# Performance work log

Measured on AMD Instinct MI355X. Metric: run time of the kernel, lower is better.

## Reference

```python
import jax, jax.numpy as jnp
import numpy as np

B = 8192          # batch (tokens)
D_LAT = 1024      # latent_dim
D_EMB = 1024      # embed_dim
D = D_LAT + D_EMB # input_dim = 2048
E = 8             # num_experts
K = 2             # top-k


def setup_inputs() -> dict:
    key = jax.random.key(0)
    ks = jax.random.split(key, 6)
    s = 1.0 / np.sqrt(D)  # PyTorch nn.Linear init bound
    return {
        "x": jax.random.normal(ks[0], (B, D_LAT), dtype=jnp.float32),
        "y": jax.random.normal(ks[1], (B, D_EMB), dtype=jnp.float32),
        # expert Linear weights [E, out=D, in=D] and biases [E, D]
        "W_experts": jax.random.uniform(ks[2], (E, D, D), jnp.float32, -s, s),
        "b_experts": jax.random.uniform(ks[3], (E, D), jnp.float32, -s, s),
        # gate Linear weight [E, D] and bias [E]
        "W_gate": jax.random.uniform(ks[4], (E, D), jnp.float32, -s, s),
        "b_gate": jax.random.uniform(ks[5], (E,), jnp.float32, -s, s),
    }


def reference(x, y, W_experts, b_experts, W_gate, b_gate):
    # inp: [B, D]
    inp = jnp.concatenate([x, y], axis=1)
    # gating (eval mode: no noise): [B, E]
    gate_logits = inp @ W_gate.T + b_gate
    # top-k values/indices (sorted descending, matching torch.topk): [B, K]
    topk_val, topk_idx = jax.lax.top_k(gate_logits, K)
    topk_gates = jax.nn.softmax(topk_val, axis=1)  # [B, K]
    # dense all-expert outputs, matching original per-expert loop: [B, E, D]
    all_out = jnp.einsum('bd,eod->beo', inp, W_experts) + b_experts[None, :, :]
    # gather top-k expert outputs: [B, K, D]
    topk_out = jnp.take_along_axis(all_out, topk_idx[:, :, None], axis=1)
    # gate-weighted combine: [B, D]
    fused = jnp.sum(topk_out * topk_gates[:, :, None], axis=1)
    return fused
```

## Files before the change

kernel.cpp:

```cpp
#include <hip/hip_runtime.h>
#include <stdint.h>

typedef __attribute__((ext_vector_type(4))) float f32x4;
typedef __attribute__((ext_vector_type(8))) short short8v;
typedef __attribute__((ext_vector_type(8))) unsigned short ushort8v;
typedef __attribute__((ext_vector_type(4))) unsigned short ushort4v;

#define NB 8192
#define ND 2048
#define NE 8
#define NT 32

__device__ __forceinline__ unsigned short f2bf(float f) {
    union { float f; uint32_t u; } c; c.f = f;
    uint32_t u = c.u;
    u = u + 0x7FFFu + ((u >> 16) & 1u);
    return (unsigned short)(u >> 16);
}

__global__ __launch_bounds__(256) void cvt_w_kernel(const float* __restrict__ W,
                                                    unsigned short* __restrict__ Wb) {
    size_t i = ((size_t)blockIdx.x * 256 + threadIdx.x) * 8;
    float4 a = *(const float4*)(W + i);
    float4 b = *(const float4*)(W + i + 4);
    ushort8v o;
    o[0] = f2bf(a.x); o[1] = f2bf(a.y); o[2] = f2bf(a.z); o[3] = f2bf(a.w);
    o[4] = f2bf(b.x); o[5] = f2bf(b.y); o[6] = f2bf(b.z); o[7] = f2bf(b.w);
    *(ushort8v*)(Wb + i) = o;
}

__global__ __launch_bounds__(256) void gatecvt_kernel(const float* __restrict__ x,
                                                      const float* __restrict__ y,
                                                      const float* __restrict__ Wg,
                                                      const float* __restrict__ bg,
                                                      unsigned short* __restrict__ inpb,
                                                      int* __restrict__ tkidx,
                                                      float* __restrict__ tkg) {
    const int wave = threadIdx.x >> 6, lane = threadIdx.x & 63;
    const int b = blockIdx.x * 4 + wave;
    const float* xb = x + (size_t)b * 1024;
    const float* yb = y + (size_t)b * 1024;
    unsigned short* ob = inpb + (size_t)b * ND;
    double acc[NE] = {0, 0, 0, 0, 0, 0, 0, 0};
#pragma unroll
    for (int it = 0; it < 8; it++) {
        const int d = it * 256 + lane * 4;
        float4 v = (it < 4) ? *(const float4*)(xb + d) : *(const float4*)(yb + (d - 1024));
        ushort4v o;
        o[0] = f2bf(v.x); o[1] = f2bf(v.y); o[2] = f2bf(v.z); o[3] = f2bf(v.w);
        *(ushort4v*)(ob + d) = o;
#pragma unroll
        for (int e = 0; e < NE; e++) {
            float4 w = *(const float4*)(Wg + e * ND + d);
            acc[e] += (double)v.x * (double)w.x + (double)v.y * (double)w.y
                    + (double)v.z * (double)w.z + (double)v.w * (double)w.w;
        }
    }
#pragma unroll
    for (int e = 0; e < NE; e++) {
        double s = acc[e];
#pragma unroll
        for (int o = 32; o >= 1; o >>= 1) s += __shfl_xor(s, o, 64);
        acc[e] = s;
    }
    if (lane == 0) {
        double v0 = -1e300, v1 = -1e300; int i0 = 0, i1 = 1;
#pragma unroll
        for (int e = 0; e < NE; e++) {
            double val = acc[e] + (double)bg[e];
            if (val > v0)      { v1 = v0; i1 = i0; v0 = val; i0 = e; }
            else if (val > v1) { v1 = val; i1 = e; }
        }
        double e1 = exp(v1 - v0);
        double inv = 1.0 / (1.0 + e1);
        tkidx[b * 2]     = i0;
        tkidx[b * 2 + 1] = i1;
        tkg[b * 2]       = (float)inv;
        tkg[b * 2 + 1]   = (float)(e1 * inv);
    }
}

__global__ __launch_bounds__(256) void hist_kernel(const int* __restrict__ tkidx,
                                                   int* __restrict__ hist) {
    const int p = blockIdx.x * 256 + threadIdx.x;
    const int wave = threadIdx.x >> 6, lane = threadIdx.x & 63;
    const int e = tkidx[p];
    __shared__ int cnt[4][8];
#pragma unroll
    for (int e2 = 0; e2 < 8; e2++) {
        unsigned long long m = __ballot(e == e2);
        if (lane == e2) cnt[wave][e2] = __popcll(m);
    }
    __syncthreads();
    if (threadIdx.x < 8)
        hist[blockIdx.x * 8 + threadIdx.x] =
            cnt[0][threadIdx.x] + cnt[1][threadIdx.x] + cnt[2][threadIdx.x] + cnt[3][threadIdx.x];
}

__global__ void scan_kernel(const int* __restrict__ hist, int* __restrict__ chunkbase,
                            int* __restrict__ meta) {
    __shared__ int total[8], off[8];
    const int t = threadIdx.x;
    if (t < 8) {
        int run = 0;
        for (int c = 0; c < 64; c++) { chunkbase[c * 8 + t] = run; run += hist[c * 8 + t]; }
        total[t] = run; meta[t] = run;
    }
    __syncthreads();
    if (t == 0) { int o = 0; for (int e = 0; e < 8; e++) { off[e] = o; meta[8 + e] = o; o += total[e]; } }
    __syncthreads();
    for (int i = t; i < 512; i += 64) chunkbase[i] += off[i & 7];
}

__global__ __launch_bounds__(256) void fill_kernel(const int* __restrict__ tkidx,
                                                   const float* __restrict__ tkg,
                                                   const int* __restrict__ chunkbase,
                                                   int* __restrict__ tok,
                                                   float* __restrict__ gat) {
    const int p = blockIdx.x * 256 + threadIdx.x;
    const int wave = threadIdx.x >> 6, lane = threadIdx.x & 63;
    const int e = tkidx[p];
    const float g = tkg[p];
    __shared__ int cnt[4][8];
    unsigned long long mym = 0;
#pragma unroll
    for (int e2 = 0; e2 < 8; e2++) {
        unsigned long long m = __ballot(e == e2);
        if (e == e2) mym = m;
        if (lane == e2) cnt[wave][e2] = __popcll(m);
    }
    __syncthreads();
    int basep = chunkbase[blockIdx.x * 8 + e];
    for (int w = 0; w < wave; w++) basep += cnt[w][e];
    const int rank = __popcll(mym & ((1ull << lane) - 1ull));
    tok[basep + rank] = p >> 1;
    gat[basep + rank] = g;
}

#define GLD16(gp, lp) __builtin_amdgcn_global_load_lds( \
    (const __attribute__((address_space(1))) uint32_t*)(gp), \
    (__attribute__((address_space(3))) uint32_t*)(lp), 16, 0, 0)

__global__ __launch_bounds__(512, 2) void moe_gemm_kernel(
    const unsigned short* __restrict__ Ab,
    const unsigned short* __restrict__ Wb,
    const float* __restrict__ bias,
    const int* __restrict__ tok,
    const float* __restrict__ gat,
    const int* __restrict__ meta,
    float* __restrict__ out)
{
    const int e = blockIdx.z;
    const int cnt = meta[e];
    const int row0 = blockIdx.y * 256;
    if (row0 >= cnt) return;
    const int col0 = blockIdx.x * 256;
    const int base = meta[8 + e];

    __shared__ __align__(16) unsigned short S[2][4][128][64];

    const int tid  = threadIdx.x;
    const int wv   = tid >> 6;
    const int lane = tid & 63;
    const int wr = wv >> 2, wcn = wv & 3;
    const int fr = lane & 15, kh = lane >> 4;

    const int srow = tid >> 3;
    const int cg8  = ((tid & 7) ^ (srow & 7)) * 8;
    const unsigned short* wbase = Wb + (size_t)e * ND * ND;
    const unsigned short* aptr[2][2];
    const unsigned short* bptr[2][2];
#pragma unroll
    for (int h = 0; h < 2; h++)
#pragma unroll
        for (int i = 0; i < 2; i++) {
            int rt = h * 128 + i * 64 + srow;
            int gr = row0 + rt; if (gr > cnt - 1) gr = cnt - 1;
            aptr[h][i] = Ab + (size_t)tok[base + gr] * ND + cg8;
            bptr[h][i] = wbase + (size_t)(col0 + rt) * ND + cg8;
        }

#define STAGE_A(SB, SM, SK) do { \
    GLD16(aptr[SM][0] + (SK), (char*)&S[SB][SM][0][0] + tid * 16); \
    GLD16(aptr[SM][1] + (SK), (char*)&S[SB][SM][0][0] + tid * 16 + 8192); } while (0)
#define STAGE_B(SB, SN, SK) do { \
    GLD16(bptr[SN][0] + (SK), (char*)&S[SB][2 + SN][0][0] + tid * 16); \
    GLD16(bptr[SN][1] + (SK), (char*)&S[SB][2 + SN][0][0] + tid * 16 + 8192); } while (0)

    f32x4 acc[8][4];
#pragma unroll
    for (int m = 0; m < 8; m++)
#pragma unroll
        for (int n = 0; n < 4; n++) acc[m][n] = f32x4{0.f, 0.f, 0.f, 0.f};

    const int arow = wr * 64 + fr;
    const int brow = wcn * 32 + fr;
    int ca[2];
#pragma unroll
    for (int ks = 0; ks < 2; ks++) ca[ks] = ((ks * 4 + kh) ^ (fr & 7)) * 8;

#define PHASE(PB, PM, PN, ...) do { \
    short8v ar[4][2], br[2][2]; \
    _Pragma("unroll") \
    for (int ks = 0; ks < 2; ks++) { \
        _Pragma("unroll") \
        for (int ml = 0; ml < 4; ml++) \
            ar[ml][ks] = *(const short8v*)&S[PB][PM][arow + ml * 16][ca[ks]]; \
        _Pragma("unroll") \
        for (int nl = 0; nl < 2; nl++) \
            br[nl][ks] = *(const short8v*)&S[PB][2 + PN][brow + nl * 16][ca[ks]]; \
    } \
    __VA_ARGS__; \
    __builtin_amdgcn_sched_barrier(0); \
    __builtin_amdgcn_s_barrier(); \
    asm volatile("s_waitcnt lgkmcnt(0)" ::: "memory"); \
    __builtin_amdgcn_sched_barrier(0); \
    __builtin_amdgcn_s_setprio(1); \
    _Pragma("unroll") \
    for (int ks = 0; ks < 2; ks++) \
        _Pragma("unroll") \
        for (int ml = 0; ml < 4; ml++) \
            _Pragma("unroll") \
            for (int nl = 0; nl < 2; nl++) \
                acc[PM * 4 + ml][PN * 2 + nl] = __builtin_amdgcn_mfma_f32_16x16x32_bf16( \
                    ar[ml][ks], br[nl][ks], acc[PM * 4 + ml][PN * 2 + nl], 0, 0, 0); \
    __builtin_amdgcn_s_setprio(0); \
    __builtin_amdgcn_sched_barrier(0); \
    __builtin_amdgcn_s_barrier(); \
} while (0)

    STAGE_B(0, 0, 0);
    STAGE_A(0, 0, 0);
    STAGE_A(0, 1, 0);
    STAGE_B(0, 1, 0);
    STAGE_B(1, 0, 64);
    STAGE_A(1, 0, 64);
    asm volatile("s_waitcnt vmcnt(4)" ::: "memory");
    __builtin_amdgcn_sched_barrier(0);
    __builtin_amdgcn_s_barrier();

    int buf = 0;
    for (int t = 0; t < NT; t++) {
        const int nb = buf ^ 1;
        const int kt1 = (t + 1) * 64;
        const int kt2 = (t + 2) * 64;
        PHASE(buf, 0, 0, { if (t + 1 < NT) STAGE_A(nb, 1, kt1); });
        PHASE(buf, 1, 0, { if (t + 1 < NT) STAGE_B(nb, 1, kt1); });
        PHASE(buf, 0, 1, { if (t + 2 < NT) STAGE_B(buf, 0, kt2); });
        PHASE(buf, 1, 1, { if (t + 2 < NT) STAGE_A(buf, 0, kt2); });
        if (t + 1 < NT) {
            if (t == NT - 2) asm volatile("s_waitcnt vmcnt(0)" ::: "memory");
            else             asm volatile("s_waitcnt vmcnt(6)" ::: "memory");
            __builtin_amdgcn_sched_barrier(0);
            __builtin_amdgcn_s_barrier();
        }
        buf = nb;
    }

    int   coln[4];
    float bv[4];
#pragma unroll
    for (int n = 0; n < 4; n++) {
        coln[n] = col0 + (n >> 1) * 128 + wcn * 32 + (n & 1) * 16 + fr;
        bv[n] = bias[e * ND + coln[n]];
    }
#pragma unroll
    for (int m = 0; m < 8; m++) {
        const int rbase = row0 + (m >> 2) * 128 + wr * 64 + (m & 3) * 16 + kh * 4;
#pragma unroll
        for (int j = 0; j < 4; j++) {
            const int R = rbase + j;
            if (R < cnt) {
                const int tkn = tok[base + R];
                const float g = gat[base + R];
                float* orow = out + (size_t)tkn * ND;
#pragma unroll
                for (int n = 0; n < 4; n++)
                    atomicAdd(orow + coln[n], g * (acc[m][n][j] + bv[n]));
            }
        }
    }
#undef PHASE
#undef STAGE_A
#undef STAGE_B
}

extern "C" void kernel_launch(void* const* d_in, const int* in_sizes, int n_in,
                              void* d_out, int out_size, void* d_ws, size_t ws_size,
                              hipStream_t stream) {
    const float* x  = (const float*)d_in[0];
    const float* y  = (const float*)d_in[1];
    const float* We = (const float*)d_in[2];
    const float* be = (const float*)d_in[3];
    const float* Wg = (const float*)d_in[4];
    const float* bg = (const float*)d_in[5];
    float* out = (float*)d_out;

    char* ws = (char*)d_ws;
    int*   meta  = (int*)ws;
    int*   hist  = (int*)(ws + 256);
    int*   cbase = (int*)(ws + 256 + 2048);
    int*   tkidx = (int*)(ws + 8192);
    float* tkg   = (float*)(ws + 8192 + 65536);
    int*   tok   = (int*)(ws + 8192 + 2 * 65536);
    float* gat   = (float*)(ws + 8192 + 3 * 65536);
    unsigned short* inpb = (unsigned short*)(ws + 8192 + 4 * 65536);
    unsigned short* wb   = (unsigned short*)(ws + 8192 + 4 * 65536 + (size_t)NB * ND * 2);

    (void)hipMemsetAsync(d_out, 0, (size_t)NB * ND * sizeof(float), stream);
    cvt_w_kernel<<<16384, 256, 0, stream>>>(We, wb);
    gatecvt_kernel<<<2048, 256, 0, stream>>>(x, y, Wg, bg, inpb, tkidx, tkg);
    hist_kernel<<<64, 256, 0, stream>>>(tkidx, hist);
    scan_kernel<<<1, 64, 0, stream>>>(hist, cbase, meta);
    fill_kernel<<<64, 256, 0, stream>>>(tkidx, tkg, cbase, tok, gat);
    moe_gemm_kernel<<<dim3(8, 32, 8), 512, 0, stream>>>(inpb, wb, be, tok, gat, meta, out);
}
```

Before: 358.7 us.

## Split phases by k-substep and reuse B fragments across M halves

Restructures the four-phase MFMA loop so each phase handles one k-substep over all four N fragments. The B fragments loaded in one phase are kept in registers and reused in the next phase for the other M half, cutting LDS reads of B. The global prefetch schedule and vmcnt waits change so that B is now only one tile ahead instead of two. This shortens prefetch lead time for B, which could expose global latency, and keeps more fragment registers live across phases.

```diff
diff --git a/kernel.cpp b/kernel.cpp
--- a/kernel.cpp
+++ b/kernel.cpp
@@ -194,22 +194,20 @@
         for (int n = 0; n < 4; n++) acc[m][n] = f32x4{0.f, 0.f, 0.f, 0.f};
 
     const int arow = wr * 64 + fr;
-    const int brow = wcn * 32 + fr;
     int ca[2];
 #pragma unroll
     for (int ks = 0; ks < 2; ks++) ca[ks] = ((ks * 4 + kh) ^ (fr & 7)) * 8;
 
-#define PHASE(PB, PM, PN, ...) do { \
-    short8v ar[4][2], br[2][2]; \
-    _Pragma("unroll") \
-    for (int ks = 0; ks < 2; ks++) { \
-        _Pragma("unroll") \
-        for (int ml = 0; ml < 4; ml++) \
-            ar[ml][ks] = *(const short8v*)&S[PB][PM][arow + ml * 16][ca[ks]]; \
-        _Pragma("unroll") \
-        for (int nl = 0; nl < 2; nl++) \
-            br[nl][ks] = *(const short8v*)&S[PB][2 + PN][brow + nl * 16][ca[ks]]; \
-    } \
+    short8v br[4];
+
+#define PH_FULL(PB, PM, KS, ...) do { \
+    short8v ar[4]; \
+    _Pragma("unroll") \
+    for (int ml = 0; ml < 4; ml++) \
+        ar[ml] = *(const short8v*)&S[PB][PM][arow + ml * 16][ca[KS]]; \
+    _Pragma("unroll") \
+    for (int n = 0; n < 4; n++) \
+        br[n] = *(const short8v*)&S[PB][2 + (n >> 1)][wcn * 32 + (n & 1) * 16 + fr][ca[KS]]; \
     __VA_ARGS__; \
     __builtin_amdgcn_sched_barrier(0); \
     __builtin_amdgcn_s_barrier(); \
@@ -217,25 +215,44 @@
     __builtin_amdgcn_sched_barrier(0); \
     __builtin_amdgcn_s_setprio(1); \
     _Pragma("unroll") \
-    for (int ks = 0; ks < 2; ks++) \
+    for (int ml = 0; ml < 4; ml++) \
         _Pragma("unroll") \
-        for (int ml = 0; ml < 4; ml++) \
-            _Pragma("unroll") \
-            for (int nl = 0; nl < 2; nl++) \
-                acc[PM * 4 + ml][PN * 2 + nl] = __builtin_amdgcn_mfma_f32_16x16x32_bf16( \
-                    ar[ml][ks], br[nl][ks], acc[PM * 4 + ml][PN * 2 + nl], 0, 0, 0); \
+        for (int n = 0; n < 4; n++) \
+            acc[PM * 4 + ml][n] = __builtin_amdgcn_mfma_f32_16x16x32_bf16( \
+                ar[ml], br[n], acc[PM * 4 + ml][n], 0, 0, 0); \
     __builtin_amdgcn_s_setprio(0); \
     __builtin_amdgcn_sched_barrier(0); \
     __builtin_amdgcn_s_barrier(); \
 } while (0)
 
+#define PH_REUSE(PB, PM, KS, ...) do { \
+    short8v ar[4]; \
+    _Pragma("unroll") \
+    for (int ml = 0; ml < 4; ml++) \
+        ar[ml] = *(const short8v*)&S[PB][PM][arow + ml * 16][ca[KS]]; \
+    __VA_ARGS__; \
+    __builtin_amdgcn_sched_barrier(0); \
+    __builtin_amdgcn_s_barrier(); \
+    asm volatile("s_waitcnt lgkmcnt(0)" ::: "memory"); \
+    __builtin_amdgcn_sched_barrier(0); \
+    __builtin_amdgcn_s_setprio(1); \
+    _Pragma("unroll") \
+    for (int ml = 0; ml < 4; ml++) \
+        _Pragma("unroll") \
+        for (int n = 0; n < 4; n++) \
+            acc[PM * 4 + ml][n] = __builtin_amdgcn_mfma_f32_16x16x32_bf16( \
+                ar[ml], br[n], acc[PM * 4 + ml][n], 0, 0, 0); \
+    __builtin_amdgcn_s_setprio(0); \
+    __builtin_amdgcn_sched_barrier(0); \
+    __builtin_amdgcn_s_barrier(); \
+} while (0)
+
+    STAGE_A(0, 0, 0);
     STAGE_B(0, 0, 0);
-    STAGE_A(0, 0, 0);
+    STAGE_B(0, 1, 0);
     STAGE_A(0, 1, 0);
-    STAGE_B(0, 1, 0);
-    STAGE_B(1, 0, 64);
     STAGE_A(1, 0, 64);
-    asm volatile("s_waitcnt vmcnt(4)" ::: "memory");
+    asm volatile("s_waitcnt vmcnt(2)" ::: "memory");
     __builtin_amdgcn_sched_barrier(0);
     __builtin_amdgcn_s_barrier();
 
@@ -244,13 +261,13 @@
         const int nb = buf ^ 1;
         const int kt1 = (t + 1) * 64;
         const int kt2 = (t + 2) * 64;
-        PHASE(buf, 0, 0, { if (t + 1 < NT) STAGE_A(nb, 1, kt1); });
-        PHASE(buf, 1, 0, { if (t + 1 < NT) STAGE_B(nb, 1, kt1); });
-        PHASE(buf, 0, 1, { if (t + 2 < NT) STAGE_B(buf, 0, kt2); });
-        PHASE(buf, 1, 1, { if (t + 2 < NT) STAGE_A(buf, 0, kt2); });
+        PH_FULL (buf, 0, 0, { if (t + 1 < NT) STAGE_A(nb, 1, kt1); });
+        PH_REUSE(buf, 1, 0, { if (t + 1 < NT) STAGE_B(nb, 0, kt1); });
+        PH_FULL (buf, 0, 1, { if (t + 1 < NT) STAGE_B(nb, 1, kt1); });
+        PH_REUSE(buf, 1, 1, { if (t + 2 < NT) STAGE_A(buf, 0, kt2); });
         if (t + 1 < NT) {
             if (t == NT - 2) asm volatile("s_waitcnt vmcnt(0)" ::: "memory");
-            else             asm volatile("s_waitcnt vmcnt(6)" ::: "memory");
+            else             asm volatile("s_waitcnt vmcnt(2)" ::: "memory");
             __builtin_amdgcn_sched_barrier(0);
             __builtin_amdgcn_s_barrier();
         }
@@ -280,7 +297,8 @@
             }
         }
     }
-#undef PHASE
+#undef PH_FULL
+#undef PH_REUSE
 #undef STAGE_A
 #undef STAGE_B
 }
```

After: 334.0 us. -6.9%, faster.
